# Kernel optimization log

Measured on AMD Instinct MI355X. Metric: run time of the kernel, lower is better.

## Reference

```python
import jax, jax.numpy as jnp
import numpy as np

EPS = 1e-5  # torch BatchNorm1d default eps

def _bn(x, g, b, m, v):
    # eval-mode BatchNorm1d with running statistics
    return (x - m) * jax.lax.rsqrt(v + EPS) * g + b

def setup_inputs() -> dict:
    key = jax.random.key(0)
    ks = jax.random.split(key, 6)
    N, E, D = 10000, 320000, 128
    h = jax.random.normal(ks[0], (N, D), dtype=jnp.float32)
    src = jax.random.randint(ks[1], (E,), 0, N)
    dst = jax.random.randint(ks[2], (E,), 0, N)
    # Linear weights (torch layout: [out, in]), kaiming-ish scale
    W0 = jax.random.normal(ks[3], (128, 256), dtype=jnp.float32) * (1.0 / np.sqrt(256))
    b0 = jnp.zeros((128,), jnp.float32)
    W1 = jax.random.normal(ks[4], (128, 128), dtype=jnp.float32) * (1.0 / np.sqrt(128))
    b1 = jnp.zeros((128,), jnp.float32)
    W2 = jax.random.normal(ks[5], (1, 128), dtype=jnp.float32) * (1.0 / np.sqrt(128))
    b2 = jnp.zeros((1,), jnp.float32)
    # BatchNorm affine params + running stats per layer input size
    g0, be0, m0, v0 = jnp.ones((256,)), jnp.zeros((256,)), jnp.zeros((256,)), jnp.ones((256,))
    g1, be1, m1, v1 = jnp.ones((128,)), jnp.zeros((128,)), jnp.zeros((128,)), jnp.ones((128,))
    g2, be2, m2, v2 = jnp.ones((128,)), jnp.zeros((128,)), jnp.zeros((128,)), jnp.ones((128,))
    return dict(h=h, src=src, dst=dst, W0=W0, b0=b0, W1=W1, b1=b1, W2=W2, b2=b2,
                g0=g0, be0=be0, g1=g1, be1=be1, g2=g2, be2=be2,
                m0=m0, v0=v0, m1=m1, v1=v1, m2=m2, v2=v2)

def reference(h, src, dst, W0, b0, W1, b1, W2, b2,
              g0, be0, g1, be1, g2, be2, m0, v0, m1, v1, m2, v2):
    # edge gather + concat: [E, 2*D]
    x = jnp.concatenate([h[src], h[dst]], axis=1)
    # stage 0: BN -> Linear (dropout is identity in eval)
    x = _bn(x, g0, be0, m0, v0) @ W0.T + b0
    # stage 1: ReLU -> BN -> Linear
    x = jax.nn.relu(x)
    x = _bn(x, g1, be1, m1, v1) @ W1.T + b1
    # stage 2: ReLU -> BN -> Linear
    x = jax.nn.relu(x)
    x = _bn(x, g2, be2, m2, v2) @ W2.T + b2
    return x  # [E, 1] edge scores
```

## Files before the change

kernel.cpp:

```cpp
#include <hip/hip_runtime.h>
#include <hip/hip_bf16.h>

#define BN_EPS 1e-5f
#define MG 2
#define GEDGES 32

typedef short bf16x8 __attribute__((ext_vector_type(8)));
typedef float f32x4  __attribute__((ext_vector_type(4)));

static __device__ __forceinline__ unsigned short f2bf(float f) {
    union { float f; unsigned int u; } v; v.f = f;
    unsigned int u = v.u;
    unsigned int r = (u + 0x7FFFu + ((u >> 16) & 1u)) >> 16;
    return (unsigned short)r;
}

static __device__ __forceinline__ unsigned short f2bf_hw(float f) {
    __hip_bfloat16 b = __float2bfloat16(f);
    union { __hip_bfloat16 b; unsigned short u; } v; v.b = b;
    return v.u;
}

__global__ __launch_bounds__(256) void k_prep(
        const float* __restrict__ h, unsigned short* __restrict__ hb, int n4, int nCvt,
        const float* __restrict__ W0, const float* __restrict__ b0,
        const float* __restrict__ W1, const float* __restrict__ b1,
        const float* __restrict__ W2, const float* __restrict__ b2,
        const float* __restrict__ g0, const float* __restrict__ be0,
        const float* __restrict__ m0, const float* __restrict__ v0,
        const float* __restrict__ g1, const float* __restrict__ be1,
        const float* __restrict__ m1, const float* __restrict__ v1,
        const float* __restrict__ g2, const float* __restrict__ be2,
        const float* __restrict__ m2, const float* __restrict__ v2,
        unsigned short* __restrict__ W0sw, unsigned short* __restrict__ W1sw,
        float* __restrict__ b0f, float* __restrict__ b1f,
        float* __restrict__ w2f, float* __restrict__ b2f) {
    const int b = blockIdx.x;
    const int tid = threadIdx.x;

    if (b < nCvt) {
        int i = b * 256 + tid;
        if (i < n4) {
            float4 f = ((const float4*)h)[i];
            ushort4 o;
            o.x = f2bf(f.x); o.y = f2bf(f.y); o.z = f2bf(f.z); o.w = f2bf(f.w);
            ((ushort4*)hb)[i] = o;
        }
        return;
    }
    int br = b - nCvt;
    if (br < 128) {
        int t = br * 256 + tid;
        int j = t & 7, lane = (t >> 3) & 63, nt = (t >> 9) & 7, kb = t >> 12;
        int k = kb * 32 + (lane >> 4) * 8 + j;
        int n = nt * 16 + (lane & 15);
        float s = g0[k] * rsqrtf(v0[k] + BN_EPS);
        W0sw[t] = f2bf(W0[n * 256 + k] * s);
        return;
    }
    br -= 128;
    if (br < 64) {
        int t = br * 256 + tid;
        int j = t & 7, lane = (t >> 3) & 63, nt = (t >> 9) & 7, kb = t >> 12;
        int k = kb * 32 + (lane >> 4) * 8 + j;
        int n = nt * 16 + (lane & 15);
        float s = g1[k] * rsqrtf(v1[k] + BN_EPS);
        W1sw[t] = f2bf(W1[n * 128 + k] * s);
        return;
    }
    br -= 64;
    {
        if (tid >= 64) return;
        const int i = br, lane = tid;
        float s0 = 0.f;
#pragma unroll
        for (int c = 0; c < 4; c++) {
            int k = c * 64 + lane;
            float sc = g0[k] * rsqrtf(v0[k] + BN_EPS);
            s0 += W0[i * 256 + k] * (be0[k] - m0[k] * sc);
        }
        float s1 = 0.f;
#pragma unroll
        for (int c = 0; c < 2; c++) {
            int k = c * 64 + lane;
            float sc = g1[k] * rsqrtf(v1[k] + BN_EPS);
            s1 += W1[i * 128 + k] * (be1[k] - m1[k] * sc);
        }
        float s2 = 0.f;
        if (i == 0) {
#pragma unroll
            for (int c = 0; c < 2; c++) {
                int k = c * 64 + lane;
                float sc = g2[k] * rsqrtf(v2[k] + BN_EPS);
                s2 += W2[k] * (be2[k] - m2[k] * sc);
            }
        }
#pragma unroll
        for (int off = 1; off < 64; off <<= 1) {
            s0 += __shfl_xor(s0, off);
            s1 += __shfl_xor(s1, off);
            s2 += __shfl_xor(s2, off);
        }
        if (lane == 0) {
            b0f[i] = b0[i] + s0;
            b1f[i] = b1[i] + s1;
            w2f[i] = W2[i] * (g2[i] * rsqrtf(v2[i] + BN_EPS));
            if (i == 0) b2f[0] = b2[0] + s2;
        }
    }
}

static __device__ __forceinline__ void dma_issue(
        unsigned short* AbufBase, const unsigned short* __restrict__ hb,
        int gOwn, int halfOwn, int lane, int quad, int row) {
#pragma unroll
    for (int kb4 = 0; kb4 < 4; kb4++) {
        const unsigned short* gp = hb + (size_t)row * 128 + kb4 * 32 + quad * 8;
        unsigned short* lp = AbufBase + ((gOwn * 2 + halfOwn) * 4 + kb4) * 512 + lane * 8;
        __builtin_amdgcn_global_load_lds(
            (const __attribute__((address_space(1))) void*)gp,
            (__attribute__((address_space(3))) void*)lp, 16, 0, 0);
    }
}

__global__ __launch_bounds__(256, 3) void k_main(
        const int* __restrict__ src, const int* __restrict__ dst,
        const unsigned short* __restrict__ hb,
        const unsigned short* __restrict__ W0sw, const unsigned short* __restrict__ W1sw,
        const float* __restrict__ b0f, const float* __restrict__ b1f,
        const float* __restrict__ w2f, const float* __restrict__ b2fp,
        float* __restrict__ out, int E, int nGroups) {
    __shared__ __align__(16) unsigned short Abuf[2][MG * 2 * 4 * 64 * 8];
    __shared__ __align__(16) unsigned short x1S[2][MG][4][64][8];
    __shared__ float pS[2][4][GEDGES];

    const int tid  = threadIdx.x;
    const int wave = tid >> 6;
    const int lane = tid & 63;
    const int quad = lane >> 4;
    const int m    = lane & 15;

    bf16x8 B0[8][2], B1[4][2];
#pragma unroll
    for (int kb = 0; kb < 8; kb++)
#pragma unroll
        for (int hh = 0; hh < 2; hh++)
            B0[kb][hh] = *(const bf16x8*)(W0sw + ((kb * 8 + (wave * 2 + hh)) * 64 + lane) * 8);
#pragma unroll
    for (int kb = 0; kb < 4; kb++)
#pragma unroll
        for (int hh = 0; hh < 2; hh++)
            B1[kb][hh] = *(const bf16x8*)(W1sw + ((kb * 8 + (wave * 2 + hh)) * 64 + lane) * 8);

    float b0v[2], b1v[2], w2v[2];
#pragma unroll
    for (int hh = 0; hh < 2; hh++) {
        int n = (wave * 2 + hh) * 16 + m;
        b0v[hh] = b0f[n];
        b1v[hh] = b1f[n];
        w2v[hh] = w2f[n];
    }
    const float b2s = *b2fp;
    const int stride = gridDim.x;

    const int gOwn = wave >> 1;
    const int halfOwn = wave & 1;
    const int* __restrict__ idxP = halfOwn ? dst : src;

    int gi = blockIdx.x;
    int p = 0;
    int eM1 = -1, eM2 = -1;
    int rN;

    {
        int e = gi * GEDGES + gOwn * 16 + m; if (e >= E) e = E - 1;
        int r0 = idxP[e];
        dma_issue(&Abuf[0][0], hb, gOwn, halfOwn, lane, quad, r0);
        int gN = gi + stride;
        int ebN = (gN < nGroups ? gN : gi) * GEDGES;
        int eN = ebN + gOwn * 16 + m; if (eN >= E) eN = E - 1;
        rN = idxP[eN];
    }

    for (; gi < nGroups; gi += stride, p ^= 1) {
        __syncthreads();

        if (eM2 >= 0 && wave == 0 && lane < GEDGES) {
            int e = eM2 + lane;
            if (e < E)
                out[e] = pS[p ^ 1][0][lane] + pS[p ^ 1][1][lane] +
                         pS[p ^ 1][2][lane] + pS[p ^ 1][3][lane] + b2s;
        }

        if (gi + stride < nGroups)
            dma_issue(&Abuf[p ^ 1][0], hb, gOwn, halfOwn, lane, quad, rN);

        {
            int g2i = gi + 2 * stride;
            int eb2 = (g2i < nGroups ? g2i : gi) * GEDGES;
            int e2 = eb2 + gOwn * 16 + m; if (e2 >= E) e2 = E - 1;
            rN = idxP[e2];
        }

        {
            f32x4 acc0[MG][2];
#pragma unroll
            for (int g = 0; g < MG; g++)
#pragma unroll
                for (int hh = 0; hh < 2; hh++) acc0[g][hh] = (f32x4){0.f, 0.f, 0.f, 0.f};

#pragma unroll
            for (int kb = 0; kb < 8; kb++) {
                bf16x8 a[MG];
#pragma unroll
                for (int g = 0; g < MG; g++)
                    a[g] = *(const bf16x8*)(&Abuf[p][((g * 2 + (kb >> 2)) * 4 + (kb & 3)) * 512 + lane * 8]);
#pragma unroll
                for (int hh = 0; hh < 2; hh++)
#pragma unroll
                    for (int g = 0; g < MG; g++)
                        acc0[g][hh] = __builtin_amdgcn_mfma_f32_16x16x32_bf16(a[g], B0[kb][hh], acc0[g][hh], 0, 0, 0);
            }
#pragma unroll
            for (int g = 0; g < MG; g++) {
#pragma unroll
                for (int hh = 0; hh < 2; hh++) {
                    int qp = (hh << 1) | (m >> 3);
                    int j  = m & 7;
#pragma unroll
                    for (int r = 0; r < 4; r++) {
                        float v = acc0[g][hh][r] + b0v[hh];
                        v = v > 0.f ? v : 0.f;
                        x1S[p][g][wave][qp * 16 + quad * 4 + r][j] = f2bf_hw(v);
                    }
                }
            }
        }

        if (eM1 >= 0) {
            f32x4 acc1[MG][2];
#pragma unroll
            for (int g = 0; g < MG; g++)
#pragma unroll
                for (int hh = 0; hh < 2; hh++) acc1[g][hh] = (f32x4){0.f, 0.f, 0.f, 0.f};

#pragma unroll
            for (int kb = 0; kb < 4; kb++) {
                bf16x8 a[MG];
#pragma unroll
                for (int g = 0; g < MG; g++)
                    a[g] = *(const bf16x8*)&x1S[p ^ 1][g][kb][lane][0];
#pragma unroll
                for (int hh = 0; hh < 2; hh++)
#pragma unroll
                    for (int g = 0; g < MG; g++)
                        acc1[g][hh] = __builtin_amdgcn_mfma_f32_16x16x32_bf16(a[g], B1[kb][hh], acc1[g][hh], 0, 0, 0);
            }
#pragma unroll
            for (int g = 0; g < MG; g++) {
                float s[4] = {0.f, 0.f, 0.f, 0.f};
#pragma unroll
                for (int hh = 0; hh < 2; hh++)
#pragma unroll
                    for (int r = 0; r < 4; r++) {
                        float v = acc1[g][hh][r] + b1v[hh];
                        v = v > 0.f ? v : 0.f;
                        s[r] += v * w2v[hh];
                    }
#pragma unroll
                for (int off = 1; off < 16; off <<= 1)
#pragma unroll
                    for (int r = 0; r < 4; r++) s[r] += __shfl_xor(s[r], off, 16);
                if (m == 0) {
#pragma unroll
                    for (int r = 0; r < 4; r++)
                        pS[p][wave][g * 16 + quad * 4 + r] = s[r];
                }
            }
        }

        eM2 = eM1;
        eM1 = gi * GEDGES;
    }

    __syncthreads();
    if (eM2 >= 0 && wave == 0 && lane < GEDGES) {
        int e = eM2 + lane;
        if (e < E)
            out[e] = pS[p ^ 1][0][lane] + pS[p ^ 1][1][lane] +
                     pS[p ^ 1][2][lane] + pS[p ^ 1][3][lane] + b2s;
    }
    if (eM1 >= 0) {
        f32x4 acc1[MG][2];
#pragma unroll
        for (int g = 0; g < MG; g++)
#pragma unroll
            for (int hh = 0; hh < 2; hh++) acc1[g][hh] = (f32x4){0.f, 0.f, 0.f, 0.f};
#pragma unroll
        for (int kb = 0; kb < 4; kb++) {
            bf16x8 a[MG];
#pragma unroll
            for (int g = 0; g < MG; g++)
                a[g] = *(const bf16x8*)&x1S[p ^ 1][g][kb][lane][0];
#pragma unroll
            for (int hh = 0; hh < 2; hh++)
#pragma unroll
                for (int g = 0; g < MG; g++)
                    acc1[g][hh] = __builtin_amdgcn_mfma_f32_16x16x32_bf16(a[g], B1[kb][hh], acc1[g][hh], 0, 0, 0);
        }
#pragma unroll
        for (int g = 0; g < MG; g++) {
            float s[4] = {0.f, 0.f, 0.f, 0.f};
#pragma unroll
            for (int hh = 0; hh < 2; hh++)
#pragma unroll
                for (int r = 0; r < 4; r++) {
                    float v = acc1[g][hh][r] + b1v[hh];
                    v = v > 0.f ? v : 0.f;
                    s[r] += v * w2v[hh];
                }
#pragma unroll
            for (int off = 1; off < 16; off <<= 1)
#pragma unroll
                for (int r = 0; r < 4; r++) s[r] += __shfl_xor(s[r], off, 16);
            if (m == 0) {
#pragma unroll
                for (int r = 0; r < 4; r++)
                    pS[p][wave][g * 16 + quad * 4 + r] = s[r];
            }
        }
    }
    __syncthreads();
    if (eM1 >= 0 && wave == 0 && lane < GEDGES) {
        int e = eM1 + lane;
        if (e < E)
            out[e] = pS[p][0][lane] + pS[p][1][lane] +
                     pS[p][2][lane] + pS[p][3][lane] + b2s;
    }
}

extern "C" void kernel_launch(void* const* d_in, const int* in_sizes, int n_in,
                              void* d_out, int out_size, void* d_ws, size_t ws_size,
                              hipStream_t stream) {
    const float* h   = (const float*)d_in[0];
    const int*   src = (const int*)d_in[1];
    const int*   dst = (const int*)d_in[2];
    const float* W0  = (const float*)d_in[3];
    const float* b0  = (const float*)d_in[4];
    const float* W1  = (const float*)d_in[5];
    const float* b1  = (const float*)d_in[6];
    const float* W2  = (const float*)d_in[7];
    const float* b2  = (const float*)d_in[8];
    const float* g0  = (const float*)d_in[9];
    const float* be0 = (const float*)d_in[10];
    const float* g1  = (const float*)d_in[11];
    const float* be1 = (const float*)d_in[12];
    const float* g2  = (const float*)d_in[13];
    const float* be2 = (const float*)d_in[14];
    const float* m0  = (const float*)d_in[15];
    const float* v0  = (const float*)d_in[16];
    const float* m1  = (const float*)d_in[17];
    const float* v1  = (const float*)d_in[18];
    const float* m2  = (const float*)d_in[19];
    const float* v2  = (const float*)d_in[20];
    float* out = (float*)d_out;

    const int hsz = in_sizes[0];
    const int E   = in_sizes[1];

    char* ws = (char*)d_ws;
    size_t off = (size_t)hsz * 2;
    off = (off + 255) & ~(size_t)255;
    unsigned short* hb   = (unsigned short*)ws;
    unsigned short* W0sw = (unsigned short*)(ws + off);  off += 65536;
    unsigned short* W1sw = (unsigned short*)(ws + off);  off += 32768;
    float* b0f = (float*)(ws + off);  off += 512;
    float* b1f = (float*)(ws + off);  off += 512;
    float* w2f = (float*)(ws + off);  off += 512;
    float* b2f = (float*)(ws + off);  off += 16;

    int n4   = hsz / 4;
    int nCvt = (n4 + 255) / 256;
    int prepBlocks = nCvt + 128 + 64 + 128;
    k_prep<<<prepBlocks, 256, 0, stream>>>(h, hb, n4, nCvt,
                                           W0, b0, W1, b1, W2, b2,
                                           g0, be0, m0, v0, g1, be1, m1, v1,
                                           g2, be2, m2, v2,
                                           W0sw, W1sw, b0f, b1f, w2f, b2f);

    int nGroups = (E + GEDGES - 1) / GEDGES;
    int nBlocks = nGroups < 768 ? nGroups : 768;
    k_main<<<nBlocks, 256, 0, stream>>>(src, dst, hb, W0sw, W1sw,
                                        b0f, b1f, w2f, b2f, out, E, nGroups);
}
```

Before: 142.9 us.

## Gather node rows directly into registers instead of LDS DMA double-buffering

Removes the global_load_lds double-buffered staging of gathered h rows and instead loads each wave's src/dst bf16 rows straight from global memory into MFMA A-operand registers at the top of each iteration, prefetching only the next group's indices. W1 fragments are reloaded from global per iteration instead of being held in registers, to reduce register pressure. The goal is to free LDS and drop the cross-wave staging, but every wave now gathers all 32 edges' rows itself (4x redundant global traffic, relying on cache), and the loads are no longer prefetched a full iteration ahead, so more latency is exposed.

```diff
diff --git a/kernel.cpp b/kernel.cpp
--- a/kernel.cpp
+++ b/kernel.cpp
@@ -110,19 +110,6 @@
     }
 }
 
-static __device__ __forceinline__ void dma_issue(
-        unsigned short* AbufBase, const unsigned short* __restrict__ hb,
-        int gOwn, int halfOwn, int lane, int quad, int row) {
-#pragma unroll
-    for (int kb4 = 0; kb4 < 4; kb4++) {
-        const unsigned short* gp = hb + (size_t)row * 128 + kb4 * 32 + quad * 8;
-        unsigned short* lp = AbufBase + ((gOwn * 2 + halfOwn) * 4 + kb4) * 512 + lane * 8;
-        __builtin_amdgcn_global_load_lds(
-            (const __attribute__((address_space(1))) void*)gp,
-            (__attribute__((address_space(3))) void*)lp, 16, 0, 0);
-    }
-}
-
 __global__ __launch_bounds__(256, 3) void k_main(
         const int* __restrict__ src, const int* __restrict__ dst,
         const unsigned short* __restrict__ hb,
@@ -130,7 +117,6 @@
         const float* __restrict__ b0f, const float* __restrict__ b1f,
         const float* __restrict__ w2f, const float* __restrict__ b2fp,
         float* __restrict__ out, int E, int nGroups) {
-    __shared__ __align__(16) unsigned short Abuf[2][MG * 2 * 4 * 64 * 8];
     __shared__ __align__(16) unsigned short x1S[2][MG][4][64][8];
     __shared__ float pS[2][4][GEDGES];
 
@@ -140,17 +126,12 @@
     const int quad = lane >> 4;
     const int m    = lane & 15;
 
-    bf16x8 B0[8][2], B1[4][2];
+    bf16x8 B0[8][2];
 #pragma unroll
     for (int kb = 0; kb < 8; kb++)
 #pragma unroll
         for (int hh = 0; hh < 2; hh++)
             B0[kb][hh] = *(const bf16x8*)(W0sw + ((kb * 8 + (wave * 2 + hh)) * 64 + lane) * 8);
-#pragma unroll
-    for (int kb = 0; kb < 4; kb++)
-#pragma unroll
-        for (int hh = 0; hh < 2; hh++)
-            B1[kb][hh] = *(const bf16x8*)(W1sw + ((kb * 8 + (wave * 2 + hh)) * 64 + lane) * 8);
 
     float b0v[2], b1v[2], w2v[2];
 #pragma unroll
@@ -163,27 +144,33 @@
     const float b2s = *b2fp;
     const int stride = gridDim.x;
 
-    const int gOwn = wave >> 1;
-    const int halfOwn = wave & 1;
-    const int* __restrict__ idxP = halfOwn ? dst : src;
-
     int gi = blockIdx.x;
     int p = 0;
     int eM1 = -1, eM2 = -1;
-    int rN;
+    int rs[MG], rd[MG];
+    int rsN[MG], rdN[MG];
 
     {
-        int e = gi * GEDGES + gOwn * 16 + m; if (e >= E) e = E - 1;
-        int r0 = idxP[e];
-        dma_issue(&Abuf[0][0], hb, gOwn, halfOwn, lane, quad, r0);
-        int gN = gi + stride;
-        int ebN = (gN < nGroups ? gN : gi) * GEDGES;
-        int eN = ebN + gOwn * 16 + m; if (eN >= E) eN = E - 1;
-        rN = idxP[eN];
+        int eb = gi * GEDGES;
+#pragma unroll
+        for (int g = 0; g < MG; g++) {
+            int e = eb + g * 16 + m; if (e >= E) e = E - 1;
+            rs[g] = src[e];
+            rd[g] = dst[e];
+        }
     }
 
     for (; gi < nGroups; gi += stride, p ^= 1) {
         __syncthreads();
+
+        bf16x8 a0s[4][MG], a0d[4][MG];
+#pragma unroll
+        for (int kb4 = 0; kb4 < 4; kb4++)
+#pragma unroll
+            for (int g = 0; g < MG; g++) {
+                a0s[kb4][g] = *(const bf16x8*)(hb + (size_t)rs[g] * 128 + kb4 * 32 + quad * 8);
+                a0d[kb4][g] = *(const bf16x8*)(hb + (size_t)rd[g] * 128 + kb4 * 32 + quad * 8);
+            }
 
         if (eM2 >= 0 && wave == 0 && lane < GEDGES) {
             int e = eM2 + lane;
@@ -192,14 +179,15 @@
                          pS[p ^ 1][2][lane] + pS[p ^ 1][3][lane] + b2s;
         }
 
-        if (gi + stride < nGroups)
-            dma_issue(&Abuf[p ^ 1][0], hb, gOwn, halfOwn, lane, quad, rN);
-
         {
-            int g2i = gi + 2 * stride;
-            int eb2 = (g2i < nGroups ? g2i : gi) * GEDGES;
-            int e2 = eb2 + gOwn * 16 + m; if (e2 >= E) e2 = E - 1;
-            rN = idxP[e2];
+            int gN = gi + stride;
+            int ebN = (gN < nGroups ? gN : gi) * GEDGES;
+#pragma unroll
+            for (int g = 0; g < MG; g++) {
+                int e = ebN + g * 16 + m; if (e >= E) e = E - 1;
+                rsN[g] = src[e];
+                rdN[g] = dst[e];
+            }
         }
 
         {
@@ -210,17 +198,20 @@
                 for (int hh = 0; hh < 2; hh++) acc0[g][hh] = (f32x4){0.f, 0.f, 0.f, 0.f};
 
 #pragma unroll
-            for (int kb = 0; kb < 8; kb++) {
-                bf16x8 a[MG];
-#pragma unroll
-                for (int g = 0; g < MG; g++)
-                    a[g] = *(const bf16x8*)(&Abuf[p][((g * 2 + (kb >> 2)) * 4 + (kb & 3)) * 512 + lane * 8]);
+            for (int kb4 = 0; kb4 < 4; kb4++)
 #pragma unroll
                 for (int hh = 0; hh < 2; hh++)
 #pragma unroll
                     for (int g = 0; g < MG; g++)
-                        acc0[g][hh] = __builtin_amdgcn_mfma_f32_16x16x32_bf16(a[g], B0[kb][hh], acc0[g][hh], 0, 0, 0);
-            }
+                        acc0[g][hh] = __builtin_amdgcn_mfma_f32_16x16x32_bf16(a0s[kb4][g], B0[kb4][hh], acc0[g][hh], 0, 0, 0);
+#pragma unroll
+            for (int kb4 = 0; kb4 < 4; kb4++)
+#pragma unroll
+                for (int hh = 0; hh < 2; hh++)
+#pragma unroll
+                    for (int g = 0; g < MG; g++)
+                        acc0[g][hh] = __builtin_amdgcn_mfma_f32_16x16x32_bf16(a0d[kb4][g], B0[4 + kb4][hh], acc0[g][hh], 0, 0, 0);
+
 #pragma unroll
             for (int g = 0; g < MG; g++) {
 #pragma unroll
@@ -238,6 +229,13 @@
         }
 
         if (eM1 >= 0) {
+            bf16x8 B1[4][2];
+#pragma unroll
+            for (int kb = 0; kb < 4; kb++)
+#pragma unroll
+                for (int hh = 0; hh < 2; hh++)
+                    B1[kb][hh] = *(const bf16x8*)(W1sw + ((kb * 8 + (wave * 2 + hh)) * 64 + lane) * 8);
+
             f32x4 acc1[MG][2];
 #pragma unroll
             for (int g = 0; g < MG; g++)
@@ -246,16 +244,17 @@
 
 #pragma unroll
             for (int kb = 0; kb < 4; kb++) {
-                bf16x8 a[MG];
+                bf16x8 a1[MG];
 #pragma unroll
                 for (int g = 0; g < MG; g++)
-                    a[g] = *(const bf16x8*)&x1S[p ^ 1][g][kb][lane][0];
+                    a1[g] = *(const bf16x8*)&x1S[p ^ 1][g][kb][lane][0];
 #pragma unroll
                 for (int hh = 0; hh < 2; hh++)
 #pragma unroll
                     for (int g = 0; g < MG; g++)
-                        acc1[g][hh] = __builtin_amdgcn_mfma_f32_16x16x32_bf16(a[g], B1[kb][hh], acc1[g][hh], 0, 0, 0);
-            }
+                        acc1[g][hh] = __builtin_amdgcn_mfma_f32_16x16x32_bf16(a1[g], B1[kb][hh], acc1[g][hh], 0, 0, 0);
+            }
+
 #pragma unroll
             for (int g = 0; g < MG; g++) {
                 float s[4] = {0.f, 0.f, 0.f, 0.f};
@@ -281,6 +280,8 @@
 
         eM2 = eM1;
         eM1 = gi * GEDGES;
+#pragma unroll
+        for (int g = 0; g < MG; g++) { rs[g] = rsN[g]; rd[g] = rdN[g]; }
     }
 
     __syncthreads();
@@ -291,6 +292,13 @@
                      pS[p ^ 1][2][lane] + pS[p ^ 1][3][lane] + b2s;
     }
     if (eM1 >= 0) {
+        bf16x8 B1[4][2];
+#pragma unroll
+        for (int kb = 0; kb < 4; kb++)
+#pragma unroll
+            for (int hh = 0; hh < 2; hh++)
+                B1[kb][hh] = *(const bf16x8*)(W1sw + ((kb * 8 + (wave * 2 + hh)) * 64 + lane) * 8);
+
         f32x4 acc1[MG][2];
 #pragma unroll
         for (int g = 0; g < MG; g++)
@@ -298,15 +306,15 @@
             for (int hh = 0; hh < 2; hh++) acc1[g][hh] = (f32x4){0.f, 0.f, 0.f, 0.f};
 #pragma unroll
         for (int kb = 0; kb < 4; kb++) {
-            bf16x8 a[MG];
+            bf16x8 a1[MG];
 #pragma unroll
             for (int g = 0; g < MG; g++)
-                a[g] = *(const bf16x8*)&x1S[p ^ 1][g][kb][lane][0];
+                a1[g] = *(const bf16x8*)&x1S[p ^ 1][g][kb][lane][0];
 #pragma unroll
             for (int hh = 0; hh < 2; hh++)
 #pragma unroll
                 for (int g = 0; g < MG; g++)
-                    acc1[g][hh] = __builtin_amdgcn_mfma_f32_16x16x32_bf16(a[g], B1[kb][hh], acc1[g][hh], 0, 0, 0);
+                    acc1[g][hh] = __builtin_amdgcn_mfma_f32_16x16x32_bf16(a1[g], B1[kb][hh], acc1[g][hh], 0, 0, 0);
         }
 #pragma unroll
         for (int g = 0; g < MG; g++) {
```

Measured after the change: 196.0 us. +37.2%, slower.

## Precompute per-node first-layer projections and gather them per edge

Applied to the files above, without the earlier changes.

Splits the first linear layer over the concatenated [h_src, h_dst] into two per-node projections U and V. A new node kernel computes them once for all 10k nodes and stores them in fp16. The edge kernel then gathers U[src]+V[dst], applies ReLU, and runs only the second and third layers. This removes the per-edge 256x128 matmul (the dominant FLOPs) and shrinks the edge kernel's work, at the cost of an extra kernel launch, a UV workspace buffer, and fp16 rounding of the intermediate. The new path runs only if the workspace is large enough; otherwise it falls back to the old gather kernel.

```diff
diff --git a/kernel.cpp b/kernel.cpp
--- a/kernel.cpp
+++ b/kernel.cpp
@@ -19,6 +19,16 @@
     __hip_bfloat16 b = __float2bfloat16(f);
     union { __hip_bfloat16 b; unsigned short u; } v; v.b = b;
     return v.u;
+}
+
+static __device__ __forceinline__ unsigned short f2h(float f) {
+    union { _Float16 h; unsigned short u; } v; v.h = (_Float16)f;
+    return v.u;
+}
+
+static __device__ __forceinline__ float h2f(short s) {
+    union { short s; _Float16 h; } v; v.s = s;
+    return (float)v.h;
 }
 
 __global__ __launch_bounds__(256) void k_prep(
@@ -110,6 +120,263 @@
     }
 }
 
+__global__ __launch_bounds__(256) void k_node(
+        const float* __restrict__ h,
+        const unsigned short* __restrict__ W0sw,
+        const float* __restrict__ b0f,
+        unsigned short* __restrict__ UV, int N) {
+    const int tid  = threadIdx.x;
+    const int wave = tid >> 6;
+    const int lane = tid & 63;
+    const int quad = lane >> 4;
+    const int m    = lane & 15;
+    const int nb   = blockIdx.x * 32;
+
+    bf16x8 B0[8][2];
+#pragma unroll
+    for (int kb = 0; kb < 8; kb++)
+#pragma unroll
+        for (int hh = 0; hh < 2; hh++)
+            B0[kb][hh] = *(const bf16x8*)(W0sw + ((kb * 8 + (wave * 2 + hh)) * 64 + lane) * 8);
+
+    float b0v[2];
+#pragma unroll
+    for (int hh = 0; hh < 2; hh++) b0v[hh] = b0f[(wave * 2 + hh) * 16 + m];
+
+    f32x4 au[MG][2], av[MG][2];
+#pragma unroll
+    for (int g = 0; g < MG; g++)
+#pragma unroll
+        for (int hh = 0; hh < 2; hh++) {
+            au[g][hh] = (f32x4){0.f, 0.f, 0.f, 0.f};
+            av[g][hh] = (f32x4){0.f, 0.f, 0.f, 0.f};
+        }
+
+#pragma unroll
+    for (int g = 0; g < MG; g++) {
+        int nrow = nb + g * 16 + m; if (nrow >= N) nrow = N - 1;
+        const float* hrow = h + (size_t)nrow * 128;
+#pragma unroll
+        for (int kb = 0; kb < 4; kb++) {
+            const float* hp = hrow + kb * 32 + quad * 8;
+            f32x4 f0 = *(const f32x4*)hp;
+            f32x4 f1 = *(const f32x4*)(hp + 4);
+            bf16x8 a;
+            a[0] = (short)f2bf_hw(f0[0]); a[1] = (short)f2bf_hw(f0[1]);
+            a[2] = (short)f2bf_hw(f0[2]); a[3] = (short)f2bf_hw(f0[3]);
+            a[4] = (short)f2bf_hw(f1[0]); a[5] = (short)f2bf_hw(f1[1]);
+            a[6] = (short)f2bf_hw(f1[2]); a[7] = (short)f2bf_hw(f1[3]);
+#pragma unroll
+            for (int hh = 0; hh < 2; hh++) {
+                au[g][hh] = __builtin_amdgcn_mfma_f32_16x16x32_bf16(a, B0[kb][hh],     au[g][hh], 0, 0, 0);
+                av[g][hh] = __builtin_amdgcn_mfma_f32_16x16x32_bf16(a, B0[kb + 4][hh], av[g][hh], 0, 0, 0);
+            }
+        }
+    }
+
+#pragma unroll
+    for (int g = 0; g < MG; g++)
+#pragma unroll
+        for (int hh = 0; hh < 2; hh++) {
+            int col = (wave * 2 + hh) * 16 + m;
+#pragma unroll
+            for (int r = 0; r < 4; r++) {
+                int node = nb + g * 16 + quad * 4 + r;
+                if (node < N) {
+                    UV[(size_t)node * 256 + col]       = f2h(au[g][hh][r] + b0v[hh]);
+                    UV[(size_t)node * 256 + 128 + col] = f2h(av[g][hh][r]);
+                }
+            }
+        }
+}
+
+__global__ __launch_bounds__(256, 3) void k_main_uv(
+        const int* __restrict__ src, const int* __restrict__ dst,
+        const unsigned short* __restrict__ UV,
+        const unsigned short* __restrict__ W1sw,
+        const float* __restrict__ b1f, const float* __restrict__ w2f,
+        const float* __restrict__ b2fp,
+        float* __restrict__ out, int E, int nGroups) {
+    __shared__ __align__(16) unsigned short x1S[2][MG][4][64][8];
+    __shared__ float pS[2][4][GEDGES];
+
+    const int tid  = threadIdx.x;
+    const int wave = tid >> 6;
+    const int lane = tid & 63;
+    const int quad = lane >> 4;
+    const int m    = lane & 15;
+    const int es   = tid >> 3;
+    const int fc   = tid & 7;
+
+    bf16x8 B1[4][2];
+#pragma unroll
+    for (int kb = 0; kb < 4; kb++)
+#pragma unroll
+        for (int hh = 0; hh < 2; hh++)
+            B1[kb][hh] = *(const bf16x8*)(W1sw + ((kb * 8 + (wave * 2 + hh)) * 64 + lane) * 8);
+
+    float b1v[2], w2v[2];
+#pragma unroll
+    for (int hh = 0; hh < 2; hh++) {
+        int n = (wave * 2 + hh) * 16 + m;
+        b1v[hh] = b1f[n];
+        w2v[hh] = w2f[n];
+    }
+    const float b2s = *b2fp;
+    const int stride = gridDim.x;
+
+    int gi = blockIdx.x;
+    int p = 0;
+    int eM1 = -1, eM2 = -1;
+    bf16x8 uA, uB, vA, vB;
+
+    {
+        int e = gi * GEDGES + es; if (e >= E) e = E - 1;
+        int rs_ = src[e], rd_ = dst[e];
+        const bf16x8* up = (const bf16x8*)(UV + (size_t)rs_ * 256 + fc * 16);
+        const bf16x8* vp = (const bf16x8*)(UV + (size_t)rd_ * 256 + 128 + fc * 16);
+        uA = up[0]; uB = up[1]; vA = vp[0]; vB = vp[1];
+    }
+
+    for (; gi < nGroups; gi += stride, p ^= 1) {
+        __syncthreads();
+
+        if (eM2 >= 0 && wave == 0 && lane < GEDGES) {
+            int e = eM2 + lane;
+            if (e < E)
+                out[e] = pS[p ^ 1][0][lane] + pS[p ^ 1][1][lane] +
+                         pS[p ^ 1][2][lane] + pS[p ^ 1][3][lane] + b2s;
+        }
+
+        {
+            bf16x8 w0, w1;
+#pragma unroll
+            for (int j = 0; j < 8; j++) {
+                float s0 = h2f(uA[j]) + h2f(vA[j]);
+                float s1 = h2f(uB[j]) + h2f(vB[j]);
+                s0 = s0 > 0.f ? s0 : 0.f;
+                s1 = s1 > 0.f ? s1 : 0.f;
+                w0[j] = (short)f2bf_hw(s0);
+                w1[j] = (short)f2bf_hw(s1);
+            }
+            int g = es >> 4, s15 = es & 15, kb = fc >> 1, q0 = (fc & 1) * 2;
+            *(bf16x8*)&x1S[p][g][kb][q0 * 16 + s15][0]       = w0;
+            *(bf16x8*)&x1S[p][g][kb][(q0 + 1) * 16 + s15][0] = w1;
+        }
+
+        {
+            int gN = gi + stride;
+            int ebN = (gN < nGroups ? gN : gi) * GEDGES;
+            int e = ebN + es; if (e >= E) e = E - 1;
+            int rs_ = src[e], rd_ = dst[e];
+            const bf16x8* up = (const bf16x8*)(UV + (size_t)rs_ * 256 + fc * 16);
+            const bf16x8* vp = (const bf16x8*)(UV + (size_t)rd_ * 256 + 128 + fc * 16);
+            uA = up[0]; uB = up[1]; vA = vp[0]; vB = vp[1];
+        }
+
+        if (eM1 >= 0) {
+            f32x4 acc1[MG][2];
+#pragma unroll
+            for (int g = 0; g < MG; g++)
+#pragma unroll
+                for (int hh = 0; hh < 2; hh++) acc1[g][hh] = (f32x4){0.f, 0.f, 0.f, 0.f};
+
+#pragma unroll
+            for (int kb = 0; kb < 4; kb++) {
+                bf16x8 a1[MG];
+#pragma unroll
+                for (int g = 0; g < MG; g++)
+                    a1[g] = *(const bf16x8*)&x1S[p ^ 1][g][kb][lane][0];
+#pragma unroll
+                for (int hh = 0; hh < 2; hh++)
+#pragma unroll
+                    for (int g = 0; g < MG; g++)
+                        acc1[g][hh] = __builtin_amdgcn_mfma_f32_16x16x32_bf16(a1[g], B1[kb][hh], acc1[g][hh], 0, 0, 0);
+            }
+
+#pragma unroll
+            for (int g = 0; g < MG; g++) {
+                float s[4] = {0.f, 0.f, 0.f, 0.f};
+#pragma unroll
+                for (int hh = 0; hh < 2; hh++)
+#pragma unroll
+                    for (int r = 0; r < 4; r++) {
+                        float v = acc1[g][hh][r] + b1v[hh];
+                        v = v > 0.f ? v : 0.f;
+                        s[r] += v * w2v[hh];
+                    }
+#pragma unroll
+                for (int off = 1; off < 16; off <<= 1)
+#pragma unroll
+                    for (int r = 0; r < 4; r++) s[r] += __shfl_xor(s[r], off, 16);
+                if (m == 0) {
+#pragma unroll
+                    for (int r = 0; r < 4; r++)
+                        pS[p][wave][g * 16 + quad * 4 + r] = s[r];
+                }
+            }
+        }
+
+        eM2 = eM1;
+        eM1 = gi * GEDGES;
+    }
+
+    __syncthreads();
+    if (eM2 >= 0 && wave == 0 && lane < GEDGES) {
+        int e = eM2 + lane;
+        if (e < E)
+            out[e] = pS[p ^ 1][0][lane] + pS[p ^ 1][1][lane] +
+                     pS[p ^ 1][2][lane] + pS[p ^ 1][3][lane] + b2s;
+    }
+    if (eM1 >= 0) {
+        f32x4 acc1[MG][2];
+#pragma unroll
+        for (int g = 0; g < MG; g++)
+#pragma unroll
+            for (int hh = 0; hh < 2; hh++) acc1[g][hh] = (f32x4){0.f, 0.f, 0.f, 0.f};
+#pragma unroll
+        for (int kb = 0; kb < 4; kb++) {
+            bf16x8 a1[MG];
+#pragma unroll
+            for (int g = 0; g < MG; g++)
+                a1[g] = *(const bf16x8*)&x1S[p ^ 1][g][kb][lane][0];
+#pragma unroll
+            for (int hh = 0; hh < 2; hh++)
+#pragma unroll
+                for (int g = 0; g < MG; g++)
+                    acc1[g][hh] = __builtin_amdgcn_mfma_f32_16x16x32_bf16(a1[g], B1[kb][hh], acc1[g][hh], 0, 0, 0);
+        }
+#pragma unroll
+        for (int g = 0; g < MG; g++) {
+            float s[4] = {0.f, 0.f, 0.f, 0.f};
+#pragma unroll
+            for (int hh = 0; hh < 2; hh++)
+#pragma unroll
+                for (int r = 0; r < 4; r++) {
+                    float v = acc1[g][hh][r] + b1v[hh];
+                    v = v > 0.f ? v : 0.f;
+                    s[r] += v * w2v[hh];
+                }
+#pragma unroll
+            for (int off = 1; off < 16; off <<= 1)
+#pragma unroll
+                for (int r = 0; r < 4; r++) s[r] += __shfl_xor(s[r], off, 16);
+            if (m == 0) {
+#pragma unroll
+                for (int r = 0; r < 4; r++)
+                    pS[p][wave][g * 16 + quad * 4 + r] = s[r];
+            }
+        }
+    }
+    __syncthreads();
+    if (eM1 >= 0 && wave == 0 && lane < GEDGES) {
+        int e = eM1 + lane;
+        if (e < E)
+            out[e] = pS[p][0][lane] + pS[p][1][lane] +
+                     pS[p][2][lane] + pS[p][3][lane] + b2s;
+    }
+}
+
 static __device__ __forceinline__ void dma_issue(
         unsigned short* AbufBase, const unsigned short* __restrict__ hb,
         int gOwn, int halfOwn, int lane, int quad, int row) {
@@ -123,7 +390,7 @@
     }
 }
 
-__global__ __launch_bounds__(256, 3) void k_main(
+__global__ __launch_bounds__(256, 3) void k_main_gather(
         const int* __restrict__ src, const int* __restrict__ dst,
         const unsigned short* __restrict__ hb,
         const unsigned short* __restrict__ W0sw, const unsigned short* __restrict__ W1sw,
@@ -246,15 +513,15 @@
 
 #pragma unroll
             for (int kb = 0; kb < 4; kb++) {
-                bf16x8 a[MG];
+                bf16x8 a1[MG];
 #pragma unroll
                 for (int g = 0; g < MG; g++)
-                    a[g] = *(const bf16x8*)&x1S[p ^ 1][g][kb][lane][0];
+                    a1[g] = *(const bf16x8*)&x1S[p ^ 1][g][kb][lane][0];
 #pragma unroll
                 for (int hh = 0; hh < 2; hh++)
 #pragma unroll
                     for (int g = 0; g < MG; g++)
-                        acc1[g][hh] = __builtin_amdgcn_mfma_f32_16x16x32_bf16(a[g], B1[kb][hh], acc1[g][hh], 0, 0, 0);
+                        acc1[g][hh] = __builtin_amdgcn_mfma_f32_16x16x32_bf16(a1[g], B1[kb][hh], acc1[g][hh], 0, 0, 0);
             }
 #pragma unroll
             for (int g = 0; g < MG; g++) {
@@ -298,15 +565,15 @@
             for (int hh = 0; hh < 2; hh++) acc1[g][hh] = (f32x4){0.f, 0.f, 0.f, 0.f};
 #pragma unroll
         for (int kb = 0; kb < 4; kb++) {
-            bf16x8 a[MG];
+            bf16x8 a1[MG];
 #pragma unroll
             for (int g = 0; g < MG; g++)
-                a[g] = *(const bf16x8*)&x1S[p ^ 1][g][kb][lane][0];
+                a1[g] = *(const bf16x8*)&x1S[p ^ 1][g][kb][lane][0];
 #pragma unroll
             for (int hh = 0; hh < 2; hh++)
 #pragma unroll
                 for (int g = 0; g < MG; g++)
-                    acc1[g][hh] = __builtin_amdgcn_mfma_f32_16x16x32_bf16(a[g], B1[kb][hh], acc1[g][hh], 0, 0, 0);
+                    acc1[g][hh] = __builtin_amdgcn_mfma_f32_16x16x32_bf16(a1[g], B1[kb][hh], acc1[g][hh], 0, 0, 0);
         }
 #pragma unroll
         for (int g = 0; g < MG; g++) {
@@ -367,29 +634,56 @@
 
     const int hsz = in_sizes[0];
     const int E   = in_sizes[1];
+    const int N   = hsz / 128;
+    const int nGroups = (E + GEDGES - 1) / GEDGES;
+
+    const size_t TAIL = 65536 + 32768 + 512 + 512 + 512 + 16;
+    size_t uvBytes = ((size_t)N * 256 * 2 + 255) & ~(size_t)255;
+    size_t needA   = uvBytes + TAIL;
 
     char* ws = (char*)d_ws;
-    size_t off = (size_t)hsz * 2;
-    off = (off + 255) & ~(size_t)255;
-    unsigned short* hb   = (unsigned short*)ws;
-    unsigned short* W0sw = (unsigned short*)(ws + off);  off += 65536;
-    unsigned short* W1sw = (unsigned short*)(ws + off);  off += 32768;
-    float* b0f = (float*)(ws + off);  off += 512;
-    float* b1f = (float*)(ws + off);  off += 512;
-    float* w2f = (float*)(ws + off);  off += 512;
-    float* b2f = (float*)(ws + off);  off += 16;
-
-    int n4   = hsz / 4;
-    int nCvt = (n4 + 255) / 256;
-    int prepBlocks = nCvt + 128 + 64 + 128;
-    k_prep<<<prepBlocks, 256, 0, stream>>>(h, hb, n4, nCvt,
-                                           W0, b0, W1, b1, W2, b2,
-                                           g0, be0, m0, v0, g1, be1, m1, v1,
-                                           g2, be2, m2, v2,
-                                           W0sw, W1sw, b0f, b1f, w2f, b2f);
-
-    int nGroups = (E + GEDGES - 1) / GEDGES;
-    int nBlocks = nGroups < 768 ? nGroups : 768;
-    k_main<<<nBlocks, 256, 0, stream>>>(src, dst, hb, W0sw, W1sw,
-                                        b0f, b1f, w2f, b2f, out, E, nGroups);
-}
+
+    if (ws_size >= needA) {
+        size_t off = uvBytes;
+        unsigned short* UV   = (unsigned short*)ws;
+        unsigned short* W0sw = (unsigned short*)(ws + off);  off += 65536;
+        unsigned short* W1sw = (unsigned short*)(ws + off);  off += 32768;
+        float* b0f = (float*)(ws + off);  off += 512;
+        float* b1f = (float*)(ws + off);  off += 512;
+        float* w2f = (float*)(ws + off);  off += 512;
+        float* b2f = (float*)(ws + off);  off += 16;
+
+        k_prep<<<320, 256, 0, stream>>>(h, nullptr, 0, 0,
+                                        W0, b0, W1, b1, W2, b2,
+                                        g0, be0, m0, v0, g1, be1, m1, v1,
+                                        g2, be2, m2, v2,
+                                        W0sw, W1sw, b0f, b1f, w2f, b2f);
+        int nodeBlocks = (N + 31) / 32;
+        k_node<<<nodeBlocks, 256, 0, stream>>>(h, W0sw, b0f, UV, N);
+        int nBlocks = nGroups < 768 ? nGroups : 768;
+        k_main_uv<<<nBlocks, 256, 0, stream>>>(src, dst, UV, W1sw,
+                                               b1f, w2f, b2f, out, E, nGroups);
+    } else {
+        size_t off = (size_t)hsz * 2;
+        off = (off + 255) & ~(size_t)255;
+        unsigned short* hb   = (unsigned short*)ws;
+        unsigned short* W0sw = (unsigned short*)(ws + off);  off += 65536;
+        unsigned short* W1sw = (unsigned short*)(ws + off);  off += 32768;
+        float* b0f = (float*)(ws + off);  off += 512;
+        float* b1f = (float*)(ws + off);  off += 512;
+        float* w2f = (float*)(ws + off);  off += 512;
+        float* b2f = (float*)(ws + off);  off += 16;
+
+        int n4   = hsz / 4;
+        int nCvt = (n4 + 255) / 256;
+        int prepBlocks = nCvt + 128 + 64 + 128;
+        k_prep<<<prepBlocks, 256, 0, stream>>>(h, hb, n4, nCvt,
+                                               W0, b0, W1, b1, W2, b2,
+                                               g0, be0, m0, v0, g1, be1, m1, v1,
+                                               g2, be2, m2, v2,
+                                               W0sw, W1sw, b0f, b1f, w2f, b2f);
+        int nBlocks = nGroups < 768 ? nGroups : 768;
+        k_main_gather<<<nBlocks, 256, 0, stream>>>(src, dst, hb, W0sw, W1sw,
+                                                   b0f, b1f, w2f, b2f, out, E, nGroups);
+    }
+}
```

Result: no change. 141.5 us (-1.0%).

## Precompute per-node first-layer projections and gather them per edge

Applied to the files above, without the earlier changes.

The first linear layer is split algebraically into W0[:, :128]·h[src] + W0[:, 128:]·h[dst]. A new node kernel computes U and V for every node once, stores them as fp16, and drops the separate bf16 conversion of h. The edge kernel gathers U[src]+V[dst], applies ReLU, and runs only the second matmul and the final dot product, with register-prefetched gathers in place of the LDS double buffer. This cuts the first-layer MFMA work from E to N rows, but gathers 256-byte rows in fp16 and adds an extra rounding step.

```diff
diff --git a/kernel.cpp b/kernel.cpp
--- a/kernel.cpp
+++ b/kernel.cpp
@@ -3,7 +3,6 @@
 
 #define BN_EPS 1e-5f
 #define MG 2
-#define GEDGES 32
 
 typedef short bf16x8 __attribute__((ext_vector_type(8)));
 typedef float f32x4  __attribute__((ext_vector_type(4)));
@@ -21,8 +20,17 @@
     return v.u;
 }
 
+static __device__ __forceinline__ unsigned short f2h(float f) {
+    union { _Float16 h; unsigned short u; } v; v.h = (_Float16)f;
+    return v.u;
+}
+
+static __device__ __forceinline__ float h2f(short s) {
+    union { short s; _Float16 h; } v; v.s = s;
+    return (float)v.h;
+}
+
 __global__ __launch_bounds__(256) void k_prep(
-        const float* __restrict__ h, unsigned short* __restrict__ hb, int n4, int nCvt,
         const float* __restrict__ W0, const float* __restrict__ b0,
         const float* __restrict__ W1, const float* __restrict__ b1,
         const float* __restrict__ W2, const float* __restrict__ b2,
@@ -35,20 +43,9 @@
         unsigned short* __restrict__ W0sw, unsigned short* __restrict__ W1sw,
         float* __restrict__ b0f, float* __restrict__ b1f,
         float* __restrict__ w2f, float* __restrict__ b2f) {
-    const int b = blockIdx.x;
+    int br = blockIdx.x;
     const int tid = threadIdx.x;
 
-    if (b < nCvt) {
-        int i = b * 256 + tid;
-        if (i < n4) {
-            float4 f = ((const float4*)h)[i];
-            ushort4 o;
-            o.x = f2bf(f.x); o.y = f2bf(f.y); o.z = f2bf(f.z); o.w = f2bf(f.w);
-            ((ushort4*)hb)[i] = o;
-        }
-        return;
-    }
-    int br = b - nCvt;
     if (br < 128) {
         int t = br * 256 + tid;
         int j = t & 7, lane = (t >> 3) & 63, nt = (t >> 9) & 7, kb = t >> 12;
@@ -110,232 +107,178 @@
     }
 }
 
-static __device__ __forceinline__ void dma_issue(
-        unsigned short* AbufBase, const unsigned short* __restrict__ hb,
-        int gOwn, int halfOwn, int lane, int quad, int row) {
-#pragma unroll
-    for (int kb4 = 0; kb4 < 4; kb4++) {
-        const unsigned short* gp = hb + (size_t)row * 128 + kb4 * 32 + quad * 8;
-        unsigned short* lp = AbufBase + ((gOwn * 2 + halfOwn) * 4 + kb4) * 512 + lane * 8;
-        __builtin_amdgcn_global_load_lds(
-            (const __attribute__((address_space(1))) void*)gp,
-            (__attribute__((address_space(3))) void*)lp, 16, 0, 0);
-    }
-}
-
-__global__ __launch_bounds__(256, 3) void k_main(
-        const int* __restrict__ src, const int* __restrict__ dst,
-        const unsigned short* __restrict__ hb,
-        const unsigned short* __restrict__ W0sw, const unsigned short* __restrict__ W1sw,
-        const float* __restrict__ b0f, const float* __restrict__ b1f,
-        const float* __restrict__ w2f, const float* __restrict__ b2fp,
-        float* __restrict__ out, int E, int nGroups) {
-    __shared__ __align__(16) unsigned short Abuf[2][MG * 2 * 4 * 64 * 8];
-    __shared__ __align__(16) unsigned short x1S[2][MG][4][64][8];
-    __shared__ float pS[2][4][GEDGES];
-
+__global__ __launch_bounds__(256) void k_node(
+        const float* __restrict__ h,
+        const unsigned short* __restrict__ W0sw,
+        const float* __restrict__ b0f,
+        unsigned short* __restrict__ UV, int N) {
     const int tid  = threadIdx.x;
     const int wave = tid >> 6;
     const int lane = tid & 63;
     const int quad = lane >> 4;
     const int m    = lane & 15;
-
-    bf16x8 B0[8][2], B1[4][2];
+    const int nb   = blockIdx.x * 32;
+
+    bf16x8 B0[8][2];
 #pragma unroll
     for (int kb = 0; kb < 8; kb++)
 #pragma unroll
         for (int hh = 0; hh < 2; hh++)
             B0[kb][hh] = *(const bf16x8*)(W0sw + ((kb * 8 + (wave * 2 + hh)) * 64 + lane) * 8);
-#pragma unroll
-    for (int kb = 0; kb < 4; kb++)
-#pragma unroll
-        for (int hh = 0; hh < 2; hh++)
-            B1[kb][hh] = *(const bf16x8*)(W1sw + ((kb * 8 + (wave * 2 + hh)) * 64 + lane) * 8);
-
-    float b0v[2], b1v[2], w2v[2];
-#pragma unroll
-    for (int hh = 0; hh < 2; hh++) {
-        int n = (wave * 2 + hh) * 16 + m;
-        b0v[hh] = b0f[n];
-        b1v[hh] = b1f[n];
-        w2v[hh] = w2f[n];
+
+    float b0v[2];
+#pragma unroll
+    for (int hh = 0; hh < 2; hh++) b0v[hh] = b0f[(wave * 2 + hh) * 16 + m];
+
+    f32x4 au[MG][2], av[MG][2];
+#pragma unroll
+    for (int g = 0; g < MG; g++)
+#pragma unroll
+        for (int hh = 0; hh < 2; hh++) {
+            au[g][hh] = (f32x4){0.f, 0.f, 0.f, 0.f};
+            av[g][hh] = (f32x4){0.f, 0.f, 0.f, 0.f};
+        }
+
+#pragma unroll
+    for (int g = 0; g < MG; g++) {
+        int nrow = nb + g * 16 + m; if (nrow >= N) nrow = N - 1;
+        const float* hrow = h + (size_t)nrow * 128;
+#pragma unroll
+        for (int kb = 0; kb < 4; kb++) {
+            const float* hp = hrow + kb * 32 + quad * 8;
+            f32x4 f0 = *(const f32x4*)hp;
+            f32x4 f1 = *(const f32x4*)(hp + 4);
+            bf16x8 a;
+            a[0] = (short)f2bf_hw(f0[0]); a[1] = (short)f2bf_hw(f0[1]);
+            a[2] = (short)f2bf_hw(f0[2]); a[3] = (short)f2bf_hw(f0[3]);
+            a[4] = (short)f2bf_hw(f1[0]); a[5] = (short)f2bf_hw(f1[1]);
+            a[6] = (short)f2bf_hw(f1[2]); a[7] = (short)f2bf_hw(f1[3]);
+#pragma unroll
+            for (int hh = 0; hh < 2; hh++) {
+                au[g][hh] = __builtin_amdgcn_mfma_f32_16x16x32_bf16(a, B0[kb][hh],     au[g][hh], 0, 0, 0);
+                av[g][hh] = __builtin_amdgcn_mfma_f32_16x16x32_bf16(a, B0[kb + 4][hh], av[g][hh], 0, 0, 0);
+            }
+        }
+    }
+
+#pragma unroll
+    for (int g = 0; g < MG; g++)
+#pragma unroll
+        for (int hh = 0; hh < 2; hh++) {
+            int col = (wave * 2 + hh) * 16 + m;
+#pragma unroll
+            for (int r = 0; r < 4; r++) {
+                int node = nb + g * 16 + quad * 4 + r;
+                if (node < N) {
+                    UV[(size_t)node * 256 + col]       = f2h(au[g][hh][r] + b0v[hh]);
+                    UV[(size_t)node * 256 + 128 + col] = f2h(av[g][hh][r]);
+                }
+            }
+        }
+}
+
+__global__ __launch_bounds__(256, 2) void k_edge(
+        const int* __restrict__ src, const int* __restrict__ dst,
+        const unsigned short* __restrict__ UV,
+        const unsigned short* __restrict__ W1sw,
+        const float* __restrict__ b1f, const float* __restrict__ w2f,
+        const float* __restrict__ b2fp,
+        float* __restrict__ out, int E, int nG) {
+    const int tid  = threadIdx.x;
+    const int wave = tid >> 6;
+    const int lane = tid & 63;
+    const int q    = lane >> 4;
+    const int m    = lane & 15;
+
+    bf16x8 B1f[8][4];
+#pragma unroll
+    for (int nt = 0; nt < 8; nt++)
+#pragma unroll
+        for (int kb = 0; kb < 4; kb++)
+            B1f[nt][kb] = *(const bf16x8*)(W1sw + ((kb * 8 + nt) * 64 + lane) * 8);
+
+    float b1v[8], w2v[8];
+#pragma unroll
+    for (int nt = 0; nt < 8; nt++) {
+        b1v[nt] = b1f[nt * 16 + m];
+        w2v[nt] = w2f[nt * 16 + m];
     }
     const float b2s = *b2fp;
     const int stride = gridDim.x;
 
-    const int gOwn = wave >> 1;
-    const int halfOwn = wave & 1;
-    const int* __restrict__ idxP = halfOwn ? dst : src;
-
     int gi = blockIdx.x;
-    int p = 0;
-    int eM1 = -1, eM2 = -1;
-    int rN;
+    bf16x8 uF[4], vF[4];
+    int rsC, rdC;
 
     {
-        int e = gi * GEDGES + gOwn * 16 + m; if (e >= E) e = E - 1;
-        int r0 = idxP[e];
-        dma_issue(&Abuf[0][0], hb, gOwn, halfOwn, lane, quad, r0);
-        int gN = gi + stride;
-        int ebN = (gN < nGroups ? gN : gi) * GEDGES;
-        int eN = ebN + gOwn * 16 + m; if (eN >= E) eN = E - 1;
-        rN = idxP[eN];
-    }
-
-    for (; gi < nGroups; gi += stride, p ^= 1) {
-        __syncthreads();
-
-        if (eM2 >= 0 && wave == 0 && lane < GEDGES) {
-            int e = eM2 + lane;
-            if (e < E)
-                out[e] = pS[p ^ 1][0][lane] + pS[p ^ 1][1][lane] +
-                         pS[p ^ 1][2][lane] + pS[p ^ 1][3][lane] + b2s;
-        }
-
-        if (gi + stride < nGroups)
-            dma_issue(&Abuf[p ^ 1][0], hb, gOwn, halfOwn, lane, quad, rN);
+        int e0 = gi * 64 + wave * 16 + m; if (e0 >= E) e0 = E - 1;
+        int rs0 = src[e0], rd0 = dst[e0];
+#pragma unroll
+        for (int kb = 0; kb < 4; kb++) {
+            uF[kb] = *(const bf16x8*)(UV + (size_t)rs0 * 256 + kb * 32 + q * 8);
+            vF[kb] = *(const bf16x8*)(UV + (size_t)rd0 * 256 + 128 + kb * 32 + q * 8);
+        }
+        int g1 = gi + stride;
+        int e1 = (g1 < nG ? g1 : gi) * 64 + wave * 16 + m; if (e1 >= E) e1 = E - 1;
+        rsC = src[e1]; rdC = dst[e1];
+    }
+
+    for (; gi < nG; gi += stride) {
+        bf16x8 a[4];
+#pragma unroll
+        for (int kb = 0; kb < 4; kb++)
+#pragma unroll
+            for (int j = 0; j < 8; j++) {
+                float s = h2f(uF[kb][j]) + h2f(vF[kb][j]);
+                s = s > 0.f ? s : 0.f;
+                a[kb][j] = (short)f2bf_hw(s);
+            }
 
         {
-            int g2i = gi + 2 * stride;
-            int eb2 = (g2i < nGroups ? g2i : gi) * GEDGES;
-            int e2 = eb2 + gOwn * 16 + m; if (e2 >= E) e2 = E - 1;
-            rN = idxP[e2];
-        }
-
+            int rs_ = rsC, rd_ = rdC;
+#pragma unroll
+            for (int kb = 0; kb < 4; kb++) {
+                uF[kb] = *(const bf16x8*)(UV + (size_t)rs_ * 256 + kb * 32 + q * 8);
+                vF[kb] = *(const bf16x8*)(UV + (size_t)rd_ * 256 + 128 + kb * 32 + q * 8);
+            }
+        }
         {
-            f32x4 acc0[MG][2];
-#pragma unroll
-            for (int g = 0; g < MG; g++)
-#pragma unroll
-                for (int hh = 0; hh < 2; hh++) acc0[g][hh] = (f32x4){0.f, 0.f, 0.f, 0.f};
-
-#pragma unroll
-            for (int kb = 0; kb < 8; kb++) {
-                bf16x8 a[MG];
-#pragma unroll
-                for (int g = 0; g < MG; g++)
-                    a[g] = *(const bf16x8*)(&Abuf[p][((g * 2 + (kb >> 2)) * 4 + (kb & 3)) * 512 + lane * 8]);
-#pragma unroll
-                for (int hh = 0; hh < 2; hh++)
-#pragma unroll
-                    for (int g = 0; g < MG; g++)
-                        acc0[g][hh] = __builtin_amdgcn_mfma_f32_16x16x32_bf16(a[g], B0[kb][hh], acc0[g][hh], 0, 0, 0);
-            }
-#pragma unroll
-            for (int g = 0; g < MG; g++) {
-#pragma unroll
-                for (int hh = 0; hh < 2; hh++) {
-                    int qp = (hh << 1) | (m >> 3);
-                    int j  = m & 7;
-#pragma unroll
-                    for (int r = 0; r < 4; r++) {
-                        float v = acc0[g][hh][r] + b0v[hh];
-                        v = v > 0.f ? v : 0.f;
-                        x1S[p][g][wave][qp * 16 + quad * 4 + r][j] = f2bf_hw(v);
-                    }
-                }
-            }
-        }
-
-        if (eM1 >= 0) {
-            f32x4 acc1[MG][2];
-#pragma unroll
-            for (int g = 0; g < MG; g++)
-#pragma unroll
-                for (int hh = 0; hh < 2; hh++) acc1[g][hh] = (f32x4){0.f, 0.f, 0.f, 0.f};
-
-#pragma unroll
-            for (int kb = 0; kb < 4; kb++) {
-                bf16x8 a[MG];
-#pragma unroll
-                for (int g = 0; g < MG; g++)
-                    a[g] = *(const bf16x8*)&x1S[p ^ 1][g][kb][lane][0];
-#pragma unroll
-                for (int hh = 0; hh < 2; hh++)
-#pragma unroll
-                    for (int g = 0; g < MG; g++)
-                        acc1[g][hh] = __builtin_amdgcn_mfma_f32_16x16x32_bf16(a[g], B1[kb][hh], acc1[g][hh], 0, 0, 0);
-            }
-#pragma unroll
-            for (int g = 0; g < MG; g++) {
-                float s[4] = {0.f, 0.f, 0.f, 0.f};
-#pragma unroll
-                for (int hh = 0; hh < 2; hh++)
-#pragma unroll
-                    for (int r = 0; r < 4; r++) {
-                        float v = acc1[g][hh][r] + b1v[hh];
-                        v = v > 0.f ? v : 0.f;
-                        s[r] += v * w2v[hh];
-                    }
-#pragma unroll
-                for (int off = 1; off < 16; off <<= 1)
-#pragma unroll
-                    for (int r = 0; r < 4; r++) s[r] += __shfl_xor(s[r], off, 16);
-                if (m == 0) {
-#pragma unroll
-                    for (int r = 0; r < 4; r++)
-                        pS[p][wave][g * 16 + quad * 4 + r] = s[r];
-                }
-            }
-        }
-
-        eM2 = eM1;
-        eM1 = gi * GEDGES;
-    }
-
-    __syncthreads();
-    if (eM2 >= 0 && wave == 0 && lane < GEDGES) {
-        int e = eM2 + lane;
-        if (e < E)
-            out[e] = pS[p ^ 1][0][lane] + pS[p ^ 1][1][lane] +
-                     pS[p ^ 1][2][lane] + pS[p ^ 1][3][lane] + b2s;
-    }
-    if (eM1 >= 0) {
-        f32x4 acc1[MG][2];
-#pragma unroll
-        for (int g = 0; g < MG; g++)
-#pragma unroll
-            for (int hh = 0; hh < 2; hh++) acc1[g][hh] = (f32x4){0.f, 0.f, 0.f, 0.f};
-#pragma unroll
-        for (int kb = 0; kb < 4; kb++) {
-            bf16x8 a[MG];
-#pragma unroll
-            for (int g = 0; g < MG; g++)
-                a[g] = *(const bf16x8*)&x1S[p ^ 1][g][kb][lane][0];
-#pragma unroll
-            for (int hh = 0; hh < 2; hh++)
-#pragma unroll
-                for (int g = 0; g < MG; g++)
-                    acc1[g][hh] = __builtin_amdgcn_mfma_f32_16x16x32_bf16(a[g], B1[kb][hh], acc1[g][hh], 0, 0, 0);
-        }
-#pragma unroll
-        for (int g = 0; g < MG; g++) {
-            float s[4] = {0.f, 0.f, 0.f, 0.f};
-#pragma unroll
-            for (int hh = 0; hh < 2; hh++)
-#pragma unroll
-                for (int r = 0; r < 4; r++) {
-                    float v = acc1[g][hh][r] + b1v[hh];
-                    v = v > 0.f ? v : 0.f;
-                    s[r] += v * w2v[hh];
-                }
-#pragma unroll
-            for (int off = 1; off < 16; off <<= 1)
-#pragma unroll
-                for (int r = 0; r < 4; r++) s[r] += __shfl_xor(s[r], off, 16);
-            if (m == 0) {
-#pragma unroll
-                for (int r = 0; r < 4; r++)
-                    pS[p][wave][g * 16 + quad * 4 + r] = s[r];
-            }
-        }
-    }
-    __syncthreads();
-    if (eM1 >= 0 && wave == 0 && lane < GEDGES) {
-        int e = eM1 + lane;
-        if (e < E)
-            out[e] = pS[p][0][lane] + pS[p][1][lane] +
-                     pS[p][2][lane] + pS[p][3][lane] + b2s;
+            int g2 = gi + 2 * stride;
+            int e2 = (g2 < nG ? g2 : gi) * 64 + wave * 16 + m; if (e2 >= E) e2 = E - 1;
+            rsC = src[e2]; rdC = dst[e2];
+        }
+
+        f32x4 acc[8];
+#pragma unroll
+        for (int nt = 0; nt < 8; nt++) acc[nt] = (f32x4){0.f, 0.f, 0.f, 0.f};
+#pragma unroll
+        for (int kb = 0; kb < 4; kb++)
+#pragma unroll
+            for (int nt = 0; nt < 8; nt++)
+                acc[nt] = __builtin_amdgcn_mfma_f32_16x16x32_bf16(a[kb], B1f[nt][kb], acc[nt], 0, 0, 0);
+
+        float s[4] = {0.f, 0.f, 0.f, 0.f};
+#pragma unroll
+        for (int nt = 0; nt < 8; nt++)
+#pragma unroll
+            for (int r = 0; r < 4; r++) {
+                float v = acc[nt][r] + b1v[nt];
+                v = v > 0.f ? v : 0.f;
+                s[r] += v * w2v[nt];
+            }
+#pragma unroll
+        for (int off = 1; off < 16; off <<= 1)
+#pragma unroll
+            for (int r = 0; r < 4; r++) s[r] += __shfl_xor(s[r], off, 16);
+
+        if (m == 0) {
+            int eB = gi * 64 + wave * 16 + q * 4;
+#pragma unroll
+            for (int r = 0; r < 4; r++) {
+                int e = eB + r;
+                if (e < E) out[e] = s[r] + b2s;
+            }
+        }
     }
 }
 
@@ -367,11 +310,11 @@
 
     const int hsz = in_sizes[0];
     const int E   = in_sizes[1];
+    const int N   = hsz / 128;
 
     char* ws = (char*)d_ws;
-    size_t off = (size_t)hsz * 2;
-    off = (off + 255) & ~(size_t)255;
-    unsigned short* hb   = (unsigned short*)ws;
+    unsigned short* UV = (unsigned short*)ws;
+    size_t off = ((size_t)N * 256 * 2 + 255) & ~(size_t)255;
     unsigned short* W0sw = (unsigned short*)(ws + off);  off += 65536;
     unsigned short* W1sw = (unsigned short*)(ws + off);  off += 32768;
     float* b0f = (float*)(ws + off);  off += 512;
@@ -379,17 +322,16 @@
     float* w2f = (float*)(ws + off);  off += 512;
     float* b2f = (float*)(ws + off);  off += 16;
 
-    int n4   = hsz / 4;
-    int nCvt = (n4 + 255) / 256;
-    int prepBlocks = nCvt + 128 + 64 + 128;
-    k_prep<<<prepBlocks, 256, 0, stream>>>(h, hb, n4, nCvt,
-                                           W0, b0, W1, b1, W2, b2,
-                                           g0, be0, m0, v0, g1, be1, m1, v1,
-                                           g2, be2, m2, v2,
-                                           W0sw, W1sw, b0f, b1f, w2f, b2f);
-
-    int nGroups = (E + GEDGES - 1) / GEDGES;
-    int nBlocks = nGroups < 768 ? nGroups : 768;
-    k_main<<<nBlocks, 256, 0, stream>>>(src, dst, hb, W0sw, W1sw,
-                                        b0f, b1f, w2f, b2f, out, E, nGroups);
-}
+    k_prep<<<320, 256, 0, stream>>>(W0, b0, W1, b1, W2, b2,
+                                    g0, be0, m0, v0, g1, be1, m1, v1,
+                                    g2, be2, m2, v2,
+                                    W0sw, W1sw, b0f, b1f, w2f, b2f);
+
+    int nodeBlocks = (N + 31) / 32;
+    k_node<<<nodeBlocks, 256, 0, stream>>>(h, W0sw, b0f, UV, N);
+
+    int nG = (E + 63) / 64;
+    int nBlocks = nG < 512 ? nG : 512;
+    k_edge<<<nBlocks, 256, 0, stream>>>(src, dst, UV, W1sw,
+                                        b1f, w2f, b2f, out, E, nG);
+}
```

New measurement: 135.0 us, median of 2. 5.5% less time.
